# Kernel optimization log

Measured on AMD Instinct MI355X. Metric: run time of the kernel, lower is better.

## Reference

```python
import jax, jax.numpy as jnp
import numpy as np

N, E, F, H, EF, ED, L, NL, NH, OD = 2048, 65536, 128, 512, 16, 64, 5, 4, 8, 64
MAX_DEG = 64


def _ln(x, s, b):
    m = x.mean(-1, keepdims=True)
    v = x.var(-1, keepdims=True)
    return (x - m) * jax.lax.rsqrt(v + 1e-5) * s + b


def setup_inputs() -> dict:
    key = jax.random.key(0)
    ks = jax.random.split(key, 40)
    s = 0.02
    x = jax.random.normal(ks[0], (N, F), jnp.float32)
    edge_index = jax.random.randint(ks[1], (2, E), 0, N, jnp.int32)
    edge_attr = jax.random.normal(ks[2], (E, EF), jnp.float32)
    # variable-length shortest paths, padded with -1
    plen = jax.random.randint(ks[3], (N, N), 0, L + 1, jnp.int32)
    pos = jnp.arange(L, dtype=jnp.int32)
    valid = pos[None, None, :] < plen[:, :, None]
    node_paths = jnp.where(valid, jax.random.randint(ks[4], (N, N, L), 0, N, jnp.int32), -1)
    edge_paths = jnp.where(valid, jax.random.randint(ks[5], (N, N, L), 0, E, jnp.int32), -1)
    p = {
        'x': x, 'edge_index': edge_index, 'edge_attr': edge_attr,
        'node_paths': node_paths, 'edge_paths': edge_paths,
        'W_node': s * jax.random.normal(ks[6], (F, H)), 'b_node': jnp.zeros((H,)),
        'W_edge': s * jax.random.normal(ks[7], (EF, ED)), 'b_edge': jnp.zeros((ED,)),
        'z_in': s * jax.random.normal(ks[8], (MAX_DEG, H)),
        'z_out': s * jax.random.normal(ks[9], (MAX_DEG, H)),
        'b_spatial': s * jax.random.normal(ks[10], (L,)),
        'edge_vector': s * jax.random.normal(ks[11], (L, ED)),
        'ln1_s': jnp.ones((NL, H)), 'ln1_b': jnp.zeros((NL, H)),
        'Wq': s * jax.random.normal(ks[12], (NL, H, H)), 'bq': jnp.zeros((NL, H)),
        'Wk': s * jax.random.normal(ks[13], (NL, H, H)), 'bk': jnp.zeros((NL, H)),
        'Wv': s * jax.random.normal(ks[14], (NL, H, H)), 'bv': jnp.zeros((NL, H)),
        'Wo': s * jax.random.normal(ks[15], (NL, H, H)), 'bo': jnp.zeros((NL, H)),
        'ln2_s': jnp.ones((NL, H)), 'ln2_b': jnp.zeros((NL, H)),
        'W1': s * jax.random.normal(ks[16], (NL, H, H)), 'b1': jnp.zeros((NL, H)),
        'W2': s * jax.random.normal(ks[17], (NL, H, H)), 'b2': jnp.zeros((NL, H)),
        'W_out': s * jax.random.normal(ks[18], (H, OD)), 'b_out': jnp.zeros((OD,)),
    }
    return p


def reference(x, edge_index, edge_attr, node_paths, edge_paths,
              W_node, b_node, W_edge, b_edge, z_in, z_out, b_spatial, edge_vector,
              ln1_s, ln1_b, Wq, bq, Wk, bk, Wv, bv, Wo, bo,
              ln2_s, ln2_b, W1, b1, W2, b2, W_out, b_out):
    n = x.shape[0]
    dk = H // NH
    h = x @ W_node + b_node  # [N,H]
    # centrality encoding: in/out degree -> learned embeddings, clamped
    in_deg = jnp.clip(jnp.zeros((n,), jnp.int32).at[edge_index[1]].add(1), 0, MAX_DEG - 1)
    out_deg = jnp.clip(jnp.zeros((n,), jnp.int32).at[edge_index[0]].add(1), 0, MAX_DEG - 1)
    h = h + z_in[in_deg] + z_out[out_deg]
    # edge encoding: mean over path of <edge_vector[k], edge_emb[path_k]>
    e_emb = edge_attr @ W_edge + b_edge           # [E,ED]
    w = e_emb @ edge_vector.T                     # [E,L] per-position dot products
    valid_e = edge_paths >= 0
    gath = w[jnp.clip(edge_paths, 0), jnp.arange(L)[None, None, :]]  # [N,N,L]
    cnt = valid_e.sum(-1).astype(h.dtype)
    c = jnp.where(cnt > 0, (gath * valid_e).sum(-1) / jnp.maximum(cnt, 1.0), 0.0)  # [N,N]
    # spatial encoding: learned scalar per path length
    plen = (node_paths >= 0).sum(-1)
    b_sp = jnp.where(plen > 0, b_spatial[jnp.clip(plen - 1, 0, L - 1)], 0.0)  # [N,N]
    bias = b_sp + c
    scale = 1.0 / jnp.sqrt(jnp.asarray(dk, h.dtype))
    for l in range(NL):
        y = _ln(h, ln1_s[l], ln1_b[l])
        q = (y @ Wq[l] + bq[l]).reshape(n, NH, dk)
        k = (y @ Wk[l] + bk[l]).reshape(n, NH, dk)
        v = (y @ Wv[l] + bv[l]).reshape(n, NH, dk)
        scores = jnp.einsum('ihd,jhd->hij', q, k) * scale + bias[None]
        attn = jax.nn.softmax(scores, axis=-1)
        o = jnp.einsum('hij,jhd->ihd', attn, v).reshape(n, H)
        h = h + o @ Wo[l] + bo[l]
        y2 = _ln(h, ln2_s[l], ln2_b[l])
        h = h + jax.nn.gelu(y2 @ W1[l] + b1[l]) @ W2[l] + b2[l]
    return h @ W_out + b_out
```

## Files before the change

kernel.cpp:

```cpp
#include <hip/hip_runtime.h>
#include <hip/hip_bf16.h>
#include <math.h>

#define N_NODES 2048
#define NEDGE   65536
#define FDIM    128
#define HDIM    512
#define EFD     16
#define EDD     64
#define LPATH   5
#define NLAYER  4
#define NHEAD   8
#define DK      64
#define ODIM    64
#define MAXDEG  64
#define PTOT    4194304

typedef __bf16 bf16;
typedef bf16 bf16x8 __attribute__((ext_vector_type(8)));
typedef bf16 bf16x4 __attribute__((ext_vector_type(4)));
typedef float f32x4 __attribute__((ext_vector_type(4)));
typedef unsigned short u16;

__global__ __launch_bounds__(256) void k_edge_w(const float* __restrict__ ea, const float* __restrict__ We,
                                                const float* __restrict__ be, const float* __restrict__ ev,
                                                const int* __restrict__ ei, int* __restrict__ din,
                                                int* __restrict__ dout, bf16* __restrict__ wT) {
    __shared__ float sM[80];
    __shared__ float sc[8];
    int t = threadIdx.x;
    if (t < 80) {
        int i = t / 5, j = t % 5;
        float acc = 0.f;
        for (int k = 0; k < EDD; ++k) acc += We[i * EDD + k] * ev[j * EDD + k];
        sM[t] = acc;
    } else if (t >= 128 && t < 128 + LPATH) {
        int j = t - 128;
        float acc = 0.f;
        for (int k = 0; k < EDD; ++k) acc += be[k] * ev[j * EDD + k];
        sc[j] = acc;
    }
    int e = blockIdx.x * 256 + t;
    atomicAdd(&dout[ei[e]], 1);
    atomicAdd(&din[ei[NEDGE + e]], 1);
    __syncthreads();
    const float4* p = (const float4*)(ea + (size_t)e * EFD);
    float4 a0 = p[0], a1 = p[1], a2 = p[2], a3 = p[3];
    float a[16] = {a0.x, a0.y, a0.z, a0.w, a1.x, a1.y, a1.z, a1.w,
                   a2.x, a2.y, a2.z, a2.w, a3.x, a3.y, a3.z, a3.w};
    float out[LPATH];
#pragma unroll
    for (int j = 0; j < LPATH; ++j) out[j] = sc[j];
#pragma unroll
    for (int i = 0; i < 16; ++i)
#pragma unroll
        for (int j = 0; j < LPATH; ++j) out[j] += a[i] * sM[i * LPATH + j];
#pragma unroll
    for (int j = 0; j < LPATH; ++j) wT[(size_t)j * NEDGE + e] = (bf16)out[j];
}

__global__ __launch_bounds__(1024) void k_bias3(const int* __restrict__ ep, const bf16* __restrict__ wT,
                                                const float* __restrict__ bsp, bf16* __restrict__ bias) {
    __shared__ char lds[163840];
    int t = threadIdx.x;
    size_t basep = (size_t)blockIdx.x * 8192;
    bf16x8 pre[4];
#pragma unroll
    for (int u = 0; u < 4; ++u) pre[u] = *(const bf16x8*)(wT + u * 8192 + t * 8);
    int* ish = (int*)lds;
    const int4* src = (const int4*)(ep + basep * 5);
#pragma unroll
    for (int u = 0; u < 10; ++u) ((int4*)ish)[t + 1024 * u] = src[t + 1024 * u];
    __syncthreads();
    unsigned pa[8], pb[8], pc[8];
#pragma unroll
    for (int r = 0; r < 8; ++r) {
        int p5 = (r * 1024 + t) * 5;
        int e0 = ish[p5], e1 = ish[p5 + 1], e2 = ish[p5 + 2], e3 = ish[p5 + 3], e4 = ish[p5 + 4];
        unsigned mk = (unsigned)(e0 >= 0) | ((unsigned)(e1 >= 0) << 1) | ((unsigned)(e2 >= 0) << 2)
                    | ((unsigned)(e3 >= 0) << 3) | ((unsigned)(e4 >= 0) << 4);
        pa[r] = ((unsigned)e0 & 0xFFFFu) | ((unsigned)e1 << 16);
        pb[r] = ((unsigned)e2 & 0xFFFFu) | ((unsigned)e3 << 16);
        pc[r] = ((unsigned)e4 & 0xFFFFu) | (mk << 16);
    }
    __syncthreads();
    {
        bf16* b0 = (bf16*)lds;
#pragma unroll
        for (int u = 0; u < 4; ++u) *(bf16x8*)(b0 + u * 8192 + t * 8) = pre[u];
    }
    __syncthreads();
    float csum[8] = {};
    int cur = 0;
#pragma unroll
    for (int s = 0; s < 10; ++s) {
        int l = s >> 1, half = s & 1;
        bf16x8 nxt[4];
        if (s < 9) {
            const bf16* wn = wT + (size_t)((s + 1) >> 1) * NEDGE + ((s + 1) & 1) * 32768;
#pragma unroll
            for (int u = 0; u < 4; ++u) nxt[u] = *(const bf16x8*)(wn + u * 8192 + t * 8);
        }
        const bf16* bc = (const bf16*)lds + cur * 32768;
#pragma unroll
        for (int r = 0; r < 8; ++r) {
            unsigned ix = (l == 0) ? (pa[r] & 0xFFFFu) : (l == 1) ? (pa[r] >> 16)
                        : (l == 2) ? (pb[r] & 0xFFFFu) : (l == 3) ? (pb[r] >> 16) : (pc[r] & 0xFFFFu);
            bool hit = (((pc[r] >> (16 + l)) & 1u) != 0) && ((ix >> 15) == (unsigned)half);
            if (hit) csum[r] += (float)bc[ix & 32767u];
        }
        __syncthreads();
        if (s < 9) {
            bf16* ba = (bf16*)lds + (cur ^ 1) * 32768;
#pragma unroll
            for (int u = 0; u < 4; ++u) *(bf16x8*)(ba + u * 8192 + t * 8) = nxt[u];
            cur ^= 1;
        }
        __syncthreads();
    }
#pragma unroll
    for (int r = 0; r < 8; ++r) {
        int cnt = __popc((int)((pc[r] >> 16) & 0x1Fu));
        float b = cnt ? bsp[cnt - 1] + csum[r] / (float)cnt : 0.f;
        bias[basep + r * 1024 + t] = (bf16)b;
    }
}

__global__ __launch_bounds__(256) void k_ln(const float* __restrict__ h, const float* __restrict__ sc,
                                            const float* __restrict__ bi, bf16* __restrict__ y) {
    int t = threadIdx.x, w = t >> 6, l = t & 63;
    int row = blockIdx.x * 4 + w;
    const float* hp = h + (size_t)row * HDIM + l * 8;
    float4 a = *(const float4*)hp;
    float4 b = *(const float4*)(hp + 4);
    float s = a.x + a.y + a.z + a.w + b.x + b.y + b.z + b.w;
    float q = a.x * a.x + a.y * a.y + a.z * a.z + a.w * a.w
            + b.x * b.x + b.y * b.y + b.z * b.z + b.w * b.w;
#pragma unroll
    for (int m = 1; m < 64; m <<= 1) { s += __shfl_xor(s, m); q += __shfl_xor(q, m); }
    float mean = s * (1.f / HDIM);
    float var = q * (1.f / HDIM) - mean * mean;
    float r = rsqrtf(var + 1e-5f);
    float4 s0 = *(const float4*)(sc + l * 8), s1 = *(const float4*)(sc + l * 8 + 4);
    float4 b0 = *(const float4*)(bi + l * 8), b1 = *(const float4*)(bi + l * 8 + 4);
    float va[8] = {a.x, a.y, a.z, a.w, b.x, b.y, b.z, b.w};
    float ss[8] = {s0.x, s0.y, s0.z, s0.w, s1.x, s1.y, s1.z, s1.w};
    float bb[8] = {b0.x, b0.y, b0.z, b0.w, b1.x, b1.y, b1.z, b1.w};
    bf16x8 o;
#pragma unroll
    for (int c = 0; c < 8; ++c) o[c] = (bf16)((va[c] - mean) * r * ss[c] + bb[c]);
    *(bf16x8*)(y + (size_t)row * HDIM + l * 8) = o;
}

__global__ __launch_bounds__(256) void k_wprep(const float* __restrict__ Wq, const float* __restrict__ Wk,
                                               const float* __restrict__ Wv, const float* __restrict__ Wo,
                                               const float* __restrict__ W1, const float* __restrict__ W2,
                                               const float* __restrict__ Wn, const float* __restrict__ Wout,
                                               bf16* __restrict__ Wt, bf16* __restrict__ WnT,
                                               bf16* __restrict__ WoutT) {
    __shared__ float Ls[64][68];
    int m = blockIdx.y;
    int q = blockIdx.x;
    int t = threadIdx.x;
    int rr = t >> 4, cc = t & 15;
    int nl = t >> 2, kc = t & 3;
    if (m < 24) {
        int lay = m / 6, type = m % 6;
        const float* src = type == 0 ? Wq : type == 1 ? Wk : type == 2 ? Wv : type == 3 ? Wo : type == 4 ? W1 : W2;
        src += (size_t)lay * (HDIM * HDIM);
        int tk = q >> 3, tn = q & 7;
#pragma unroll
        for (int u = 0; u < 4; ++u) {
            float4 v = *(const float4*)(src + (size_t)(tk * 64 + rr + 16 * u) * HDIM + tn * 64 + cc * 4);
            *(float4*)&Ls[rr + 16 * u][cc * 4] = v;
        }
        __syncthreads();
        bf16 tmp[16];
#pragma unroll
        for (int u = 0; u < 16; ++u) tmp[u] = (bf16)Ls[kc * 16 + u][nl];
        bf16* dst = Wt + (size_t)m * (HDIM * HDIM) + (size_t)(tn * 64 + nl) * HDIM + tk * 64 + kc * 16;
        *(bf16x8*)(dst) = *(bf16x8*)&tmp[0];
        *(bf16x8*)(dst + 8) = *(bf16x8*)&tmp[8];
    } else if (m == 24) {
        if (q >= 16) return;
        int tk = q >> 3, tn = q & 7;
#pragma unroll
        for (int u = 0; u < 4; ++u) {
            float4 v = *(const float4*)(Wn + (size_t)(tk * 64 + rr + 16 * u) * HDIM + tn * 64 + cc * 4);
            *(float4*)&Ls[rr + 16 * u][cc * 4] = v;
        }
        __syncthreads();
        bf16 tmp[16];
#pragma unroll
        for (int u = 0; u < 16; ++u) tmp[u] = (bf16)Ls[kc * 16 + u][nl];
        bf16* dst = WnT + (size_t)(tn * 64 + nl) * FDIM + tk * 64 + kc * 16;
        *(bf16x8*)dst = *(bf16x8*)&tmp[0];
        *(bf16x8*)(dst + 8) = *(bf16x8*)&tmp[8];
    } else {
        if (q >= 8) return;
        int tk = q;
#pragma unroll
        for (int u = 0; u < 4; ++u) {
            float4 v = *(const float4*)(Wout + (size_t)(tk * 64 + rr + 16 * u) * ODIM + cc * 4);
            *(float4*)&Ls[rr + 16 * u][cc * 4] = v;
        }
        __syncthreads();
        bf16 tmp[16];
#pragma unroll
        for (int u = 0; u < 16; ++u) tmp[u] = (bf16)Ls[kc * 16 + u][nl];
        bf16* dst = WoutT + (size_t)nl * HDIM + tk * 64 + kc * 16;
        *(bf16x8*)dst = *(bf16x8*)&tmp[0];
        *(bf16x8*)(dst + 8) = *(bf16x8*)&tmp[8];
    }
}

__global__ __launch_bounds__(256) void k_nmm(const float* __restrict__ x, const bf16* __restrict__ Bt,
                                             const float* __restrict__ bn, const float* __restrict__ zin,
                                             const float* __restrict__ zout, const int* __restrict__ din,
                                             const int* __restrict__ dout, float* __restrict__ h) {
    __shared__ bf16 Bs[8192];
    int t = threadIdx.x, w = t >> 6, l = t & 63, lr = l & 15, lg = l >> 4;
    int j0 = blockIdx.x * 64, i0 = blockIdx.y * 64;
    const bf16* Bp = Bt + (size_t)j0 * FDIM;
#pragma unroll
    for (int rnd = 0; rnd < 4; ++rnd) {
        int tt = rnd * 256 + t;
        int ks = tt >> 8, qq = (tt >> 6) & 3, mm = (tt >> 2) & 15, gg = tt & 3;
        *(bf16x8*)(Bs + tt * 8) = *(const bf16x8*)(Bp + (size_t)(qq * 16 + mm) * FDIM + ks * 32 + gg * 8);
    }
    __syncthreads();
    const float* ap = x + (size_t)(i0 + w * 16 + lr) * FDIM + 8 * lg;
    f32x4 acc[4] = {};
#pragma unroll
    for (int ks = 0; ks < 4; ++ks) {
        float4 f0 = *(const float4*)(ap + ks * 32);
        float4 f1 = *(const float4*)(ap + ks * 32 + 4);
        bf16x8 a;
        a[0] = (bf16)f0.x; a[1] = (bf16)f0.y; a[2] = (bf16)f0.z; a[3] = (bf16)f0.w;
        a[4] = (bf16)f1.x; a[5] = (bf16)f1.y; a[6] = (bf16)f1.z; a[7] = (bf16)f1.w;
        const bf16* bb = Bs + ks * 2048 + lr * 32 + lg * 8;
#pragma unroll
        for (int sub = 0; sub < 4; ++sub)
            acc[sub] = __builtin_amdgcn_mfma_f32_16x16x32_bf16(a, *(const bf16x8*)(bb + sub * 512), acc[sub], 0, 0, 0);
    }
#pragma unroll
    for (int r = 0; r < 4; ++r) {
        int i = i0 + w * 16 + lg * 4 + r;
        int di = min(din[i], MAXDEG - 1), dz = min(dout[i], MAXDEG - 1);
#pragma unroll
        for (int sub = 0; sub < 4; ++sub) {
            int j = j0 + sub * 16 + lr;
            h[(size_t)i * HDIM + j] = acc[sub][r] + bn[j] + zin[(size_t)di * HDIM + j] + zout[(size_t)dz * HDIM + j];
        }
    }
}

__global__ __launch_bounds__(256) void k_qkv(const bf16* __restrict__ A, const bf16* __restrict__ Wt_l,
                                             const float* __restrict__ bq, const float* __restrict__ bk,
                                             const float* __restrict__ bv, bf16* __restrict__ qf,
                                             bf16* __restrict__ kf, bf16* __restrict__ vf) {
    __shared__ bf16 Bs[16384];
    int t = threadIdx.x, w = t >> 6, l = t & 63, lr = l & 15, lg = l >> 4;
    int j0 = blockIdx.x * 32, i0 = blockIdx.y * 64;
    int type = j0 >> 9, n0 = j0 & 511;
    const bf16* Bp = Wt_l + (size_t)type * (HDIM * HDIM) + (size_t)n0 * HDIM;
#pragma unroll
    for (int rnd = 0; rnd < 8; ++rnd) {
        int tt = rnd * 256 + t;
        int ks = tt >> 7, qq = (tt >> 6) & 1, mm = (tt >> 2) & 15, gg = tt & 3;
        bf16x8 v = *(const bf16x8*)(Bp + (size_t)(qq * 16 + mm) * HDIM + ks * 32 + gg * 8);
        *(bf16x8*)(Bs + tt * 8) = v;
    }
    __syncthreads();
    const bf16* ap = A + (size_t)(i0 + w * 16 + lr) * HDIM + 8 * lg;
    const float* bvec = (type == 0 ? bq : type == 1 ? bk : bv);
    f32x4 acc[2] = {};
#pragma unroll 4
    for (int ks = 0; ks < 16; ++ks) {
        bf16x8 a  = *(const bf16x8*)(ap + ks * 32);
        const bf16* bb = Bs + ks * 1024 + lr * 32 + lg * 8;
        bf16x8 b0 = *(const bf16x8*)(bb);
        bf16x8 b1 = *(const bf16x8*)(bb + 512);
        acc[0] = __builtin_amdgcn_mfma_f32_16x16x32_bf16(a, b0, acc[0], 0, 0, 0);
        acc[1] = __builtin_amdgcn_mfma_f32_16x16x32_bf16(a, b1, acc[1], 0, 0, 0);
    }
    int h = n0 >> 6;
    if (type < 2) {
        bf16* dst = (type == 0 ? qf : kf);
        int hf = (n0 & 32) >> 5;
        float sc = (type == 0 ? 0.125f : 1.0f);
#pragma unroll
        for (int sub = 0; sub < 2; ++sub) {
#pragma unroll
            for (int r = 0; r < 4; ++r) {
                int i = i0 + w * 16 + lg * 4 + r;
                float v = (acc[sub][r] + bvec[n0 + sub * 16 + lr]) * sc;
                int lgp = sub * 2 + (lr >> 3);
                size_t off = (((size_t)(h * 128 + (i >> 4)) * 2 + hf) << 9) + lgp * 128 + (lg * 4 + r) * 8 + (lr & 7);
                dst[off] = (bf16)v;
            }
        }
    } else {
#pragma unroll
        for (int sub = 0; sub < 2; ++sub) {
#pragma unroll
            for (int r = 0; r < 4; ++r) {
                int node = i0 + w * 16 + lg * 4 + r;
                int dd = (n0 & 63) + sub * 16 + lr;
                float v = acc[sub][r] + bvec[n0 + sub * 16 + lr];
                size_t off = (((size_t)(h * 4 + (dd >> 4)) * 64 + (node >> 5)) << 9)
                           + ((node >> 3) & 3) * 128 + (dd & 15) * 8 + (node & 7);
                vf[off] = (bf16)v;
            }
        }
    }
}

#define FL_RES   1
#define FL_GELU  2
#define FL_OUTF  4

__device__ inline float gelu_f(float x) {
    float x3 = x * x * x;
    float u = 0.7978845608028654f * (x + 0.044715f * x3);
    return 0.5f * x * (1.f + tanhf(u));
}

__global__ __launch_bounds__(1024) void k_mm(const bf16* __restrict__ A, const bf16* __restrict__ Bt,
                                             const float* __restrict__ bvec, const float* __restrict__ res,
                                             float* __restrict__ outF, bf16* __restrict__ outB, int flags) {
    __shared__ bf16 Bs[32768];
    __shared__ float Osh[4][16][68];
    int t = threadIdx.x, w = t >> 6, l = t & 63, lr = l & 15, lg = l >> 4;
    int ti = w & 3, s = w >> 2;
    int j0 = blockIdx.x * 64, i0 = blockIdx.y * 64;
    const bf16* Bp = Bt + (size_t)j0 * HDIM;
#pragma unroll
    for (int rnd = 0; rnd < 4; ++rnd) {
        int tt = rnd * 1024 + t;
        int ks = tt >> 8, qq = (tt >> 6) & 3, mm = (tt >> 2) & 15, gg = tt & 3;
        bf16x8 v = *(const bf16x8*)(Bp + (size_t)(qq * 16 + mm) * HDIM + ks * 32 + gg * 8);
        *(bf16x8*)(Bs + tt * 8) = v;
    }
    __syncthreads();
    const bf16* ap = A + (size_t)(i0 + ti * 16 + lr) * HDIM + 8 * lg;
    f32x4 acc[4] = {};
#pragma unroll
    for (int kk = 0; kk < 4; ++kk) {
        int ks = s * 4 + kk;
        bf16x8 a = *(const bf16x8*)(ap + ks * 32);
        const bf16* bb = Bs + ks * 2048 + lr * 32 + lg * 8;
#pragma unroll
        for (int sub = 0; sub < 4; ++sub) {
            bf16x8 b = *(const bf16x8*)(bb + sub * 512);
            acc[sub] = __builtin_amdgcn_mfma_f32_16x16x32_bf16(a, b, acc[sub], 0, 0, 0);
        }
    }
    if (s == 0) {
#pragma unroll
        for (int sub = 0; sub < 4; ++sub)
#pragma unroll
            for (int r = 0; r < 4; ++r) Osh[ti][lg * 4 + r][sub * 16 + lr] = acc[sub][r];
    }
    __syncthreads();
    if (s == 1) {
#pragma unroll
        for (int sub = 0; sub < 4; ++sub)
#pragma unroll
            for (int r = 0; r < 4; ++r) Osh[ti][lg * 4 + r][sub * 16 + lr] += acc[sub][r];
    }
    __syncthreads();
    if (s == 2) {
#pragma unroll
        for (int sub = 0; sub < 4; ++sub)
#pragma unroll
            for (int r = 0; r < 4; ++r) Osh[ti][lg * 4 + r][sub * 16 + lr] += acc[sub][r];
    }
    __syncthreads();
    if (s == 3) {
#pragma unroll
        for (int sub = 0; sub < 4; ++sub) {
#pragma unroll
            for (int r = 0; r < 4; ++r) {
                int i = i0 + ti * 16 + lg * 4 + r;
                int j = j0 + sub * 16 + lr;
                float v = Osh[ti][lg * 4 + r][sub * 16 + lr] + acc[sub][r] + bvec[j];
                if (flags & FL_RES) v += res[(size_t)i * HDIM + j];
                if (flags & FL_GELU) v = gelu_f(v);
                if (flags & FL_OUTF) outF[(size_t)i * HDIM + j] = v;
                else outB[(size_t)i * HDIM + j] = (bf16)v;
            }
        }
    }
}

__global__ __launch_bounds__(1024) void k_mmln(const float* __restrict__ h, const bf16* __restrict__ Bt,
                                               const float* __restrict__ lnS, const float* __restrict__ lnB,
                                               const float* __restrict__ bvec, bf16* __restrict__ outB) {
    __shared__ bf16 As[32768];
    __shared__ bf16 Bs[32768];
    __shared__ float Osh[4][16][68];
    __shared__ float sbuf[HDIM], bbuf[HDIM];
    int t = threadIdx.x, w = t >> 6, l = t & 63, lr = l & 15, lg = l >> 4;
    int ti = w & 3, s = w >> 2;
    int j0 = blockIdx.x * 64, i0 = blockIdx.y * 64;
    if (t < HDIM) sbuf[t] = lnS[t];
    else bbuf[t - HDIM] = lnB[t - HDIM];
    const bf16* Bp = Bt + (size_t)j0 * HDIM;
#pragma unroll
    for (int rnd = 0; rnd < 4; ++rnd) {
        int tt = rnd * 1024 + t;
        int ks = tt >> 8, qq = (tt >> 6) & 3, mm = (tt >> 2) & 15, gg = tt & 3;
        *(bf16x8*)(Bs + tt * 8) = *(const bf16x8*)(Bp + (size_t)(qq * 16 + mm) * HDIM + ks * 32 + gg * 8);
    }
    int row = t >> 4, ksc = t & 15;
    const float* hp = h + (size_t)(i0 + row) * HDIM + ksc * 32;
    float4 hv[8];
    float S = 0.f, Q = 0.f;
#pragma unroll
    for (int u = 0; u < 8; ++u) {
        hv[u] = *(const float4*)(hp + u * 4);
        S += hv[u].x + hv[u].y + hv[u].z + hv[u].w;
        Q += hv[u].x * hv[u].x + hv[u].y * hv[u].y + hv[u].z * hv[u].z + hv[u].w * hv[u].w;
    }
#pragma unroll
    for (int m = 1; m < 16; m <<= 1) { S += __shfl_xor(S, m); Q += __shfl_xor(Q, m); }
    float mean = S * (1.f / HDIM);
    float var = Q * (1.f / HDIM) - mean * mean;
    float rr = rsqrtf(var + 1e-5f);
    float ca = rr, cc = -mean * rr;
    __syncthreads();
    {
        bf16 tmp[32];
#pragma unroll
        for (int u = 0; u < 8; ++u) {
            float vv[4] = {hv[u].x, hv[u].y, hv[u].z, hv[u].w};
#pragma unroll
            for (int c = 0; c < 4; ++c) {
                int col = ksc * 32 + u * 4 + c;
                tmp[u * 4 + c] = (bf16)(fmaf(fmaf(vv[c], ca, cc), sbuf[col], bbuf[col]));
            }
        }
        bf16* dst = As + (row >> 4) * 8192 + ksc * 512 + (row & 15) * 32;
#pragma unroll
        for (int u = 0; u < 4; ++u) *(bf16x8*)(dst + u * 8) = *(bf16x8*)&tmp[u * 8];
    }
    __syncthreads();
    const bf16* apl = As + ti * 8192 + lr * 32 + lg * 8;
    f32x4 acc[4] = {};
#pragma unroll
    for (int kk = 0; kk < 4; ++kk) {
        int ks = s * 4 + kk;
        bf16x8 a = *(const bf16x8*)(apl + ks * 512);
        const bf16* bb = Bs + ks * 2048 + lr * 32 + lg * 8;
#pragma unroll
        for (int sub = 0; sub < 4; ++sub)
            acc[sub] = __builtin_amdgcn_mfma_f32_16x16x32_bf16(a, *(const bf16x8*)(bb + sub * 512), acc[sub], 0, 0, 0);
    }
    if (s == 0) {
#pragma unroll
        for (int sub = 0; sub < 4; ++sub)
#pragma unroll
            for (int r = 0; r < 4; ++r) Osh[ti][lg * 4 + r][sub * 16 + lr] = acc[sub][r];
    }
    __syncthreads();
    if (s == 1) {
#pragma unroll
        for (int sub = 0; sub < 4; ++sub)
#pragma unroll
            for (int r = 0; r < 4; ++r) Osh[ti][lg * 4 + r][sub * 16 + lr] += acc[sub][r];
    }
    __syncthreads();
    if (s == 2) {
#pragma unroll
        for (int sub = 0; sub < 4; ++sub)
#pragma unroll
            for (int r = 0; r < 4; ++r) Osh[ti][lg * 4 + r][sub * 16 + lr] += acc[sub][r];
    }
    __syncthreads();
    if (s == 3) {
#pragma unroll
        for (int sub = 0; sub < 4; ++sub) {
#pragma unroll
            for (int r = 0; r < 4; ++r) {
                int i = i0 + ti * 16 + lg * 4 + r;
                int j = j0 + sub * 16 + lr;
                float v = gelu_f(Osh[ti][lg * 4 + r][sub * 16 + lr] + acc[sub][r] + bvec[j]);
                outB[(size_t)i * HDIM + j] = (bf16)v;
            }
        }
    }
}

__global__ __launch_bounds__(1024) void k_attn2(const bf16* __restrict__ qf, const bf16* __restrict__ kf,
                                                const bf16* __restrict__ vf, const bf16* __restrict__ biasb,
                                                bf16* __restrict__ ob) {
    __shared__ char Pb[16 * 1024];
    __shared__ float Osh[4][64][17];
    __shared__ float Msh[4][4][16], Lsh[4][4][16];
    int t = threadIdx.x, w = t >> 6, l = t & 63, lr = l & 15, lg = l >> 4;
    int ti = w & 3, s = w >> 2;
    int bid = blockIdx.x;
    int wid = (bid & 7) * 32 + (bid >> 3);
    int i0 = (wid >> 3) * 64, hh = wid & 7;
    int irow = i0 + ti * 16;

    const bf16* qb = qf + (((size_t)(hh * 128 + (irow >> 4)) * 2) << 9) + l * 8;
    bf16x8 qy0 = *(const bf16x8*)(qb);
    bf16x8 qy1 = *(const bf16x8*)(qb + 512);

    char* pwr = Pb + w * 1024 + lr * 64;
    unsigned kx = (unsigned)(lr & 6) << 3;

    float m_run = -3e38f, l_run = 0.f;
    f32x4 oacc[4] = {};

    int jb0 = s * 512;
    const bf16* kbp = kf + (((size_t)(hh * 128 + (jb0 >> 4)) * 2) << 9) + l * 8;
    bf16x8 ka0 = *(const bf16x8*)(kbp);
    bf16x8 ka1 = *(const bf16x8*)(kbp + 512);
    bf16x8 ka2 = *(const bf16x8*)(kbp + 1024);
    bf16x8 ka3 = *(const bf16x8*)(kbp + 1536);
    const bf16* bpp = biasb + (size_t)(irow + lr) * N_NODES + jb0 + lg * 4;
    bf16x4 ba0 = *(const bf16x4*)(bpp);
    bf16x4 ba1 = *(const bf16x4*)(bpp + 16);

    for (int it = 0; it < 16; ++it) {
        int jb = s * 512 + it * 32;
        const bf16* vb = vf + (((size_t)(hh * 4) * 64 + (jb >> 5)) << 9) + l * 8;
        bf16x8 vx0 = *(const bf16x8*)(vb);
        bf16x8 vx1 = *(const bf16x8*)(vb + 32768);
        bf16x8 vx2 = *(const bf16x8*)(vb + 65536);
        bf16x8 vx3 = *(const bf16x8*)(vb + 98304);
        bf16x8 kn0, kn1, kn2, kn3;
        bf16x4 bn0, bn1;
        if (it < 15) {
            int jn = jb + 32;
            const bf16* kbn = kf + (((size_t)(hh * 128 + (jn >> 4)) * 2) << 9) + l * 8;
            kn0 = *(const bf16x8*)(kbn);
            kn1 = *(const bf16x8*)(kbn + 512);
            kn2 = *(const bf16x8*)(kbn + 1024);
            kn3 = *(const bf16x8*)(kbn + 1536);
            const bf16* bpn = biasb + (size_t)(irow + lr) * N_NODES + jn + lg * 4;
            bn0 = *(const bf16x4*)(bpn);
            bn1 = *(const bf16x4*)(bpn + 16);
        }

        f32x4 s0v = {}, s1v = {};
        __builtin_amdgcn_s_setprio(1);
        s0v = __builtin_amdgcn_mfma_f32_16x16x32_bf16(ka0, qy0, s0v, 0, 0, 0);
        s0v = __builtin_amdgcn_mfma_f32_16x16x32_bf16(ka1, qy1, s0v, 0, 0, 0);
        s1v = __builtin_amdgcn_mfma_f32_16x16x32_bf16(ka2, qy0, s1v, 0, 0, 0);
        s1v = __builtin_amdgcn_mfma_f32_16x16x32_bf16(ka3, qy1, s1v, 0, 0, 0);
        __builtin_amdgcn_s_setprio(0);

        float p0[4], p1[4];
        float mt = -3e38f;
#pragma unroll
        for (int r = 0; r < 4; ++r) {
            p0[r] = s0v[r] + (float)ba0[r];
            p1[r] = s1v[r] + (float)ba1[r];
            mt = fmaxf(mt, fmaxf(p0[r], p1[r]));
        }
        mt = fmaxf(mt, __shfl_xor(mt, 16));
        mt = fmaxf(mt, __shfl_xor(mt, 32));
        if (!__all(mt <= m_run + 8.f)) {
            float mn = fmaxf(m_run, mt);
            float alpha = __expf(m_run - mn);
            l_run *= alpha;
#pragma unroll
            for (int d = 0; d < 4; ++d) oacc[d] *= alpha;
            m_run = mn;
        }
        float ps = 0.f;
        bf16x4 pk0, pk1;
#pragma unroll
        for (int r = 0; r < 4; ++r) {
            p0[r] = __expf(p0[r] - m_run);
            p1[r] = __expf(p1[r] - m_run);
            ps += p0[r] + p1[r];
            pk0[r] = (bf16)p0[r];
            pk1[r] = (bf16)p1[r];
        }
        ps += __shfl_xor(ps, 16);
        ps += __shfl_xor(ps, 32);
        l_run += ps;

        *(bf16x4*)(pwr + ((lg * 8) ^ kx)) = pk0;
        *(bf16x4*)(pwr + ((32 + lg * 8) ^ kx)) = pk1;
        asm volatile("s_waitcnt lgkmcnt(0)" ::: "memory");
        __builtin_amdgcn_sched_barrier(0x20);
        bf16x8 py = *(bf16x8*)(Pb + w * 1024 + lr * 64 + ((lg * 16) ^ kx));
        __builtin_amdgcn_s_setprio(1);
        oacc[0] = __builtin_amdgcn_mfma_f32_16x16x32_bf16(vx0, py, oacc[0], 0, 0, 0);
        oacc[1] = __builtin_amdgcn_mfma_f32_16x16x32_bf16(vx1, py, oacc[1], 0, 0, 0);
        oacc[2] = __builtin_amdgcn_mfma_f32_16x16x32_bf16(vx2, py, oacc[2], 0, 0, 0);
        oacc[3] = __builtin_amdgcn_mfma_f32_16x16x32_bf16(vx3, py, oacc[3], 0, 0, 0);
        __builtin_amdgcn_s_setprio(0);
        ka0 = kn0; ka1 = kn1; ka2 = kn2; ka3 = kn3;
        ba0 = bn0; ba1 = bn1;
    }

    __syncthreads();
    if (lg == 0) { Msh[ti][s][lr] = m_run; Lsh[ti][s][lr] = l_run; }
    __syncthreads();
    float m0 = Msh[ti][0][lr], m1 = Msh[ti][1][lr], m2 = Msh[ti][2][lr], m3 = Msh[ti][3][lr];
    float mtot = fmaxf(fmaxf(m0, m1), fmaxf(m2, m3));
    float l_tot = Lsh[ti][0][lr] * __expf(m0 - mtot) + Lsh[ti][1][lr] * __expf(m1 - mtot)
                + Lsh[ti][2][lr] * __expf(m2 - mtot) + Lsh[ti][3][lr] * __expf(m3 - mtot);
    float fac = __expf(m_run - mtot);
#pragma unroll
    for (int d = 0; d < 4; ++d) oacc[d] *= fac;
    if (s == 0) {
#pragma unroll
        for (int db = 0; db < 4; ++db)
#pragma unroll
            for (int r = 0; r < 4; ++r) Osh[ti][db * 16 + lg * 4 + r][lr] = oacc[db][r];
    }
    __syncthreads();
    if (s == 1) {
#pragma unroll
        for (int db = 0; db < 4; ++db)
#pragma unroll
            for (int r = 0; r < 4; ++r) Osh[ti][db * 16 + lg * 4 + r][lr] += oacc[db][r];
    }
    __syncthreads();
    if (s == 2) {
#pragma unroll
        for (int db = 0; db < 4; ++db)
#pragma unroll
            for (int r = 0; r < 4; ++r) Osh[ti][db * 16 + lg * 4 + r][lr] += oacc[db][r];
    }
    __syncthreads();
    if (s == 3) {
        float inv = 1.f / l_tot;
#pragma unroll
        for (int db = 0; db < 4; ++db) {
            bf16x4 o4;
#pragma unroll
            for (int r = 0; r < 4; ++r)
                o4[r] = (bf16)((Osh[ti][db * 16 + lg * 4 + r][lr] + oacc[db][r]) * inv);
            *(bf16x4*)(ob + (size_t)(irow + lr) * HDIM + hh * DK + db * 16 + lg * 4) = o4;
        }
    }
}

__global__ __launch_bounds__(256) void k_fout(const float* __restrict__ h, const bf16* __restrict__ Bt,
                                              const float* __restrict__ bvec, float* __restrict__ C) {
    __shared__ float Osh[16][68];
    int t = threadIdx.x, s = t >> 6, l = t & 63, lr = l & 15, lg = l >> 4;
    int i0 = blockIdx.x * 16;
    const float* ap = h + (size_t)(i0 + lr) * HDIM + s * 128 + lg * 8;
    f32x4 acc[4] = {};
#pragma unroll
    for (int kk = 0; kk < 4; ++kk) {
        float4 f0 = *(const float4*)(ap + kk * 32);
        float4 f1 = *(const float4*)(ap + kk * 32 + 4);
        bf16x8 a;
        a[0] = (bf16)f0.x; a[1] = (bf16)f0.y; a[2] = (bf16)f0.z; a[3] = (bf16)f0.w;
        a[4] = (bf16)f1.x; a[5] = (bf16)f1.y; a[6] = (bf16)f1.z; a[7] = (bf16)f1.w;
#pragma unroll
        for (int sub = 0; sub < 4; ++sub) {
            bf16x8 b = *(const bf16x8*)(Bt + (size_t)(sub * 16 + lr) * HDIM + s * 128 + kk * 32 + lg * 8);
            acc[sub] = __builtin_amdgcn_mfma_f32_16x16x32_bf16(a, b, acc[sub], 0, 0, 0);
        }
    }
    if (s == 0) {
#pragma unroll
        for (int sub = 0; sub < 4; ++sub)
#pragma unroll
            for (int r = 0; r < 4; ++r) Osh[lg * 4 + r][sub * 16 + lr] = acc[sub][r];
    }
    __syncthreads();
    if (s == 1) {
#pragma unroll
        for (int sub = 0; sub < 4; ++sub)
#pragma unroll
            for (int r = 0; r < 4; ++r) Osh[lg * 4 + r][sub * 16 + lr] += acc[sub][r];
    }
    __syncthreads();
    if (s == 2) {
#pragma unroll
        for (int sub = 0; sub < 4; ++sub)
#pragma unroll
            for (int r = 0; r < 4; ++r) Osh[lg * 4 + r][sub * 16 + lr] += acc[sub][r];
    }
    __syncthreads();
    if (s == 3) {
#pragma unroll
        for (int sub = 0; sub < 4; ++sub) {
#pragma unroll
            for (int r = 0; r < 4; ++r) {
                int i = i0 + lg * 4 + r;
                int j = sub * 16 + lr;
                C[(size_t)i * ODIM + j] = Osh[lg * 4 + r][sub * 16 + lr] + acc[sub][r] + bvec[j];
            }
        }
    }
}

extern "C" void kernel_launch(void* const* d_in, const int* in_sizes, int n_in,
                              void* d_out, int out_size, void* d_ws, size_t ws_size,
                              hipStream_t stream) {
    const float* x      = (const float*)d_in[0];
    const int*   ei     = (const int*)d_in[1];
    const float* eattr  = (const float*)d_in[2];
    const int*   epaths = (const int*)d_in[4];
    const float* Wn     = (const float*)d_in[5];
    const float* bn     = (const float*)d_in[6];
    const float* We     = (const float*)d_in[7];
    const float* be     = (const float*)d_in[8];
    const float* zin    = (const float*)d_in[9];
    const float* zout   = (const float*)d_in[10];
    const float* bsp    = (const float*)d_in[11];
    const float* ev     = (const float*)d_in[12];
    const float* ln1s   = (const float*)d_in[13];
    const float* ln1b   = (const float*)d_in[14];
    const float* Wq     = (const float*)d_in[15];
    const float* bq     = (const float*)d_in[16];
    const float* Wk     = (const float*)d_in[17];
    const float* bk     = (const float*)d_in[18];
    const float* Wv     = (const float*)d_in[19];
    const float* bv     = (const float*)d_in[20];
    const float* Wo     = (const float*)d_in[21];
    const float* bo     = (const float*)d_in[22];
    const float* ln2s   = (const float*)d_in[23];
    const float* ln2b   = (const float*)d_in[24];
    const float* W1     = (const float*)d_in[25];
    const float* b1     = (const float*)d_in[26];
    const float* W2     = (const float*)d_in[27];
    const float* b2     = (const float*)d_in[28];
    const float* Wout   = (const float*)d_in[29];
    const float* bout   = (const float*)d_in[30];

    char* base = (char*)d_ws;
    size_t off = 0;
    auto alloc = [&](size_t bytes) { char* p = base + off; off = (off + bytes + 255) & ~(size_t)255; return p; };
    bf16*  bias   = (bf16*)alloc((size_t)N_NODES * N_NODES * 2);
    float* h      = (float*)alloc((size_t)N_NODES * HDIM * 4);
    bf16*  wT     = (bf16*)alloc((size_t)LPATH * NEDGE * 2);
    int*   deg    = (int*)alloc(2 * N_NODES * 4);
    bf16*  WnT    = (bf16*)alloc((size_t)HDIM * FDIM * 2);
    bf16*  WoutT  = (bf16*)alloc((size_t)ODIM * HDIM * 2);
    bf16*  Wt     = (bf16*)alloc((size_t)NLAYER * 6 * HDIM * HDIM * 2);
    bf16*  y_bf   = (bf16*)alloc((size_t)N_NODES * HDIM * 2);
    bf16*  qfb    = (bf16*)alloc((size_t)NHEAD * 128 * 2 * 512 * 2);
    bf16*  kfb    = (bf16*)alloc((size_t)NHEAD * 128 * 2 * 512 * 2);
    bf16*  vfb    = (bf16*)alloc((size_t)NHEAD * 4 * 64 * 512 * 2);
    bf16*  ob_bf  = (bf16*)alloc((size_t)N_NODES * HDIM * 2);
    bf16*  t1_bf  = (bf16*)alloc((size_t)N_NODES * HDIM * 2);
    int* din = deg;
    int* dout = deg + N_NODES;

    hipMemsetAsync(deg, 0, 2 * N_NODES * sizeof(int), stream);

    k_edge_w<<<NEDGE / 256, 256, 0, stream>>>(eattr, We, be, ev, ei, din, dout, wT);
    k_bias3<<<512, 1024, 0, stream>>>(epaths, wT, bsp, bias);
    k_wprep<<<dim3(64, 26), 256, 0, stream>>>(Wq, Wk, Wv, Wo, W1, W2, Wn, Wout, Wt, WnT, WoutT);
    k_nmm<<<dim3(8, 32), 256, 0, stream>>>(x, WnT, bn, zin, zout, din, dout, h);

    dim3 gqkv(48, 32);
    dim3 gmm(8, 32);

    for (int lay = 0; lay < NLAYER; ++lay) {
        const bf16* Wt_l = Wt + (size_t)lay * 6 * HDIM * HDIM;
        size_t bOff = (size_t)lay * HDIM;
        k_ln<<<512, 256, 0, stream>>>(h, ln1s + bOff, ln1b + bOff, y_bf);
        k_qkv<<<gqkv, 256, 0, stream>>>(y_bf, Wt_l, bq + bOff, bk + bOff, bv + bOff, qfb, kfb, vfb);
        k_attn2<<<256, 1024, 0, stream>>>(qfb, kfb, vfb, bias, ob_bf);
        k_mm<<<gmm, 1024, 0, stream>>>(ob_bf, Wt_l + (size_t)3 * HDIM * HDIM, bo + bOff, h, h, nullptr, FL_RES | FL_OUTF);
        k_mmln<<<gmm, 1024, 0, stream>>>(h, Wt_l + (size_t)4 * HDIM * HDIM, ln2s + bOff, ln2b + bOff, b1 + bOff, t1_bf);
        k_mm<<<gmm, 1024, 0, stream>>>(t1_bf, Wt_l + (size_t)5 * HDIM * HDIM, b2 + bOff, h, h, nullptr, FL_RES | FL_OUTF);
    }
    k_fout<<<128, 256, 0, stream>>>(h, WoutT, bout, (float*)d_out);
}
```

Before: 462.5 us.

## Fold log2e into Q scale and bias; process two path chunks per bias block

```diff
diff --git a/kernel.cpp b/kernel.cpp
--- a/kernel.cpp
+++ b/kernel.cpp
@@ -15,6 +15,7 @@
 #define ODIM    64
 #define MAXDEG  64
 #define PTOT    4194304
+#define LOG2E   1.4426950408889634f
 
 typedef __bf16 bf16;
 typedef bf16 bf16x8 __attribute__((ext_vector_type(8)));
@@ -63,66 +64,86 @@
                                                 const float* __restrict__ bsp, bf16* __restrict__ bias) {
     __shared__ char lds[163840];
     int t = threadIdx.x;
-    size_t basep = (size_t)blockIdx.x * 8192;
-    bf16x8 pre[4];
-#pragma unroll
-    for (int u = 0; u < 4; ++u) pre[u] = *(const bf16x8*)(wT + u * 8192 + t * 8);
+    size_t basep = (size_t)blockIdx.x * 16384;
+    bf16x8 pre[8];
+#pragma unroll
+    for (int u = 0; u < 8; ++u) pre[u] = *(const bf16x8*)(wT + u * 8192 + t * 8);
     int* ish = (int*)lds;
-    const int4* src = (const int4*)(ep + basep * 5);
-#pragma unroll
-    for (int u = 0; u < 10; ++u) ((int4*)ish)[t + 1024 * u] = src[t + 1024 * u];
-    __syncthreads();
-    unsigned pa[8], pb[8], pc[8];
+    {
+        const int4* src = (const int4*)(ep + basep * 5);
+#pragma unroll
+        for (int u = 0; u < 10; ++u) ((int4*)ish)[t + 1024 * u] = src[t + 1024 * u];
+    }
+    __syncthreads();
+    unsigned pa0[8], pb0[8], pc0[8];
 #pragma unroll
     for (int r = 0; r < 8; ++r) {
         int p5 = (r * 1024 + t) * 5;
         int e0 = ish[p5], e1 = ish[p5 + 1], e2 = ish[p5 + 2], e3 = ish[p5 + 3], e4 = ish[p5 + 4];
         unsigned mk = (unsigned)(e0 >= 0) | ((unsigned)(e1 >= 0) << 1) | ((unsigned)(e2 >= 0) << 2)
                     | ((unsigned)(e3 >= 0) << 3) | ((unsigned)(e4 >= 0) << 4);
-        pa[r] = ((unsigned)e0 & 0xFFFFu) | ((unsigned)e1 << 16);
-        pb[r] = ((unsigned)e2 & 0xFFFFu) | ((unsigned)e3 << 16);
-        pc[r] = ((unsigned)e4 & 0xFFFFu) | (mk << 16);
+        pa0[r] = ((unsigned)e0 & 0xFFFFu) | ((unsigned)e1 << 16);
+        pb0[r] = ((unsigned)e2 & 0xFFFFu) | ((unsigned)e3 << 16);
+        pc0[r] = ((unsigned)e4 & 0xFFFFu) | (mk << 16);
     }
     __syncthreads();
     {
-        bf16* b0 = (bf16*)lds;
-#pragma unroll
-        for (int u = 0; u < 4; ++u) *(bf16x8*)(b0 + u * 8192 + t * 8) = pre[u];
-    }
-    __syncthreads();
-    float csum[8] = {};
-    int cur = 0;
-#pragma unroll
-    for (int s = 0; s < 10; ++s) {
-        int l = s >> 1, half = s & 1;
-        bf16x8 nxt[4];
-        if (s < 9) {
-            const bf16* wn = wT + (size_t)((s + 1) >> 1) * NEDGE + ((s + 1) & 1) * 32768;
-#pragma unroll
-            for (int u = 0; u < 4; ++u) nxt[u] = *(const bf16x8*)(wn + u * 8192 + t * 8);
-        }
-        const bf16* bc = (const bf16*)lds + cur * 32768;
+        const int4* src = (const int4*)(ep + (basep + 8192) * 5);
+#pragma unroll
+        for (int u = 0; u < 10; ++u) ((int4*)ish)[t + 1024 * u] = src[t + 1024 * u];
+    }
+    __syncthreads();
+    unsigned pa1[8], pb1[8], pc1[8];
+#pragma unroll
+    for (int r = 0; r < 8; ++r) {
+        int p5 = (r * 1024 + t) * 5;
+        int e0 = ish[p5], e1 = ish[p5 + 1], e2 = ish[p5 + 2], e3 = ish[p5 + 3], e4 = ish[p5 + 4];
+        unsigned mk = (unsigned)(e0 >= 0) | ((unsigned)(e1 >= 0) << 1) | ((unsigned)(e2 >= 0) << 2)
+                    | ((unsigned)(e3 >= 0) << 3) | ((unsigned)(e4 >= 0) << 4);
+        pa1[r] = ((unsigned)e0 & 0xFFFFu) | ((unsigned)e1 << 16);
+        pb1[r] = ((unsigned)e2 & 0xFFFFu) | ((unsigned)e3 << 16);
+        pc1[r] = ((unsigned)e4 & 0xFFFFu) | (mk << 16);
+    }
+    __syncthreads();
+    bf16* wsl = (bf16*)lds;
+#pragma unroll
+    for (int u = 0; u < 8; ++u) *(bf16x8*)(wsl + u * 8192 + t * 8) = pre[u];
+    __syncthreads();
+    float cs0[8] = {}, cs1[8] = {};
+#pragma unroll
+    for (int l = 0; l < LPATH; ++l) {
+        bf16x8 nxt[8];
+        if (l < 4) {
+            const bf16* wn = wT + (size_t)(l + 1) * NEDGE;
+#pragma unroll
+            for (int u = 0; u < 8; ++u) nxt[u] = *(const bf16x8*)(wn + u * 8192 + t * 8);
+        }
 #pragma unroll
         for (int r = 0; r < 8; ++r) {
-            unsigned ix = (l == 0) ? (pa[r] & 0xFFFFu) : (l == 1) ? (pa[r] >> 16)
-                        : (l == 2) ? (pb[r] & 0xFFFFu) : (l == 3) ? (pb[r] >> 16) : (pc[r] & 0xFFFFu);
-            bool hit = (((pc[r] >> (16 + l)) & 1u) != 0) && ((ix >> 15) == (unsigned)half);
-            if (hit) csum[r] += (float)bc[ix & 32767u];
+            unsigned ix0 = (l == 0) ? (pa0[r] & 0xFFFFu) : (l == 1) ? (pa0[r] >> 16)
+                         : (l == 2) ? (pb0[r] & 0xFFFFu) : (l == 3) ? (pb0[r] >> 16) : (pc0[r] & 0xFFFFu);
+            unsigned ix1 = (l == 0) ? (pa1[r] & 0xFFFFu) : (l == 1) ? (pa1[r] >> 16)
+                         : (l == 2) ? (pb1[r] & 0xFFFFu) : (l == 3) ? (pb1[r] >> 16) : (pc1[r] & 0xFFFFu);
+            float v0 = (float)wsl[ix0 & 0xFFFFu];
+            float v1 = (float)wsl[ix1 & 0xFFFFu];
+            cs0[r] += ((pc0[r] >> (16 + l)) & 1u) ? v0 : 0.f;
+            cs1[r] += ((pc1[r] >> (16 + l)) & 1u) ? v1 : 0.f;
         }
         __syncthreads();
-        if (s < 9) {
-            bf16* ba = (bf16*)lds + (cur ^ 1) * 32768;
-#pragma unroll
-            for (int u = 0; u < 4; ++u) *(bf16x8*)(ba + u * 8192 + t * 8) = nxt[u];
-            cur ^= 1;
+        if (l < 4) {
+#pragma unroll
+            for (int u = 0; u < 8; ++u) *(bf16x8*)(wsl + u * 8192 + t * 8) = nxt[u];
         }
         __syncthreads();
     }
 #pragma unroll
     for (int r = 0; r < 8; ++r) {
-        int cnt = __popc((int)((pc[r] >> 16) & 0x1Fu));
-        float b = cnt ? bsp[cnt - 1] + csum[r] / (float)cnt : 0.f;
-        bias[basep + r * 1024 + t] = (bf16)b;
+        int c0 = __popc((int)((pc0[r] >> 16) & 0x1Fu));
+        int c1 = __popc((int)((pc1[r] >> 16) & 0x1Fu));
+        float b0 = c0 ? (bsp[c0 - 1] + cs0[r] / (float)c0) * LOG2E : 0.f;
+        float b1 = c1 ? (bsp[c1 - 1] + cs1[r] / (float)c1) * LOG2E : 0.f;
+        bias[basep + r * 1024 + t] = (bf16)b0;
+        bias[basep + 8192 + r * 1024 + t] = (bf16)b1;
     }
 }
 
@@ -288,7 +309,7 @@
     if (type < 2) {
         bf16* dst = (type == 0 ? qf : kf);
         int hf = (n0 & 32) >> 5;
-        float sc = (type == 0 ? 0.125f : 1.0f);
+        float sc = (type == 0 ? 0.125f * LOG2E : 1.0f);
 #pragma unroll
         for (int sub = 0; sub < 2; ++sub) {
 #pragma unroll
@@ -564,9 +585,9 @@
         }
         mt = fmaxf(mt, __shfl_xor(mt, 16));
         mt = fmaxf(mt, __shfl_xor(mt, 32));
-        if (!__all(mt <= m_run + 8.f)) {
+        if (!__all(mt <= m_run + 11.5416f)) {
             float mn = fmaxf(m_run, mt);
-            float alpha = __expf(m_run - mn);
+            float alpha = exp2f(m_run - mn);
             l_run *= alpha;
 #pragma unroll
             for (int d = 0; d < 4; ++d) oacc[d] *= alpha;
@@ -576,8 +597,8 @@
         bf16x4 pk0, pk1;
 #pragma unroll
         for (int r = 0; r < 4; ++r) {
-            p0[r] = __expf(p0[r] - m_run);
-            p1[r] = __expf(p1[r] - m_run);
+            p0[r] = exp2f(p0[r] - m_run);
+            p1[r] = exp2f(p1[r] - m_run);
             ps += p0[r] + p1[r];
             pk0[r] = (bf16)p0[r];
             pk1[r] = (bf16)p1[r];
@@ -606,9 +627,9 @@
     __syncthreads();
     float m0 = Msh[ti][0][lr], m1 = Msh[ti][1][lr], m2 = Msh[ti][2][lr], m3 = Msh[ti][3][lr];
     float mtot = fmaxf(fmaxf(m0, m1), fmaxf(m2, m3));
-    float l_tot = Lsh[ti][0][lr] * __expf(m0 - mtot) + Lsh[ti][1][lr] * __expf(m1 - mtot)
-                + Lsh[ti][2][lr] * __expf(m2 - mtot) + Lsh[ti][3][lr] * __expf(m3 - mtot);
-    float fac = __expf(m_run - mtot);
+    float l_tot = Lsh[ti][0][lr] * exp2f(m0 - mtot) + Lsh[ti][1][lr] * exp2f(m1 - mtot)
+                + Lsh[ti][2][lr] * exp2f(m2 - mtot) + Lsh[ti][3][lr] * exp2f(m3 - mtot);
+    float fac = exp2f(m_run - mtot);
 #pragma unroll
     for (int d = 0; d < 4; ++d) oacc[d] *= fac;
     if (s == 0) {
@@ -755,7 +776,7 @@
     hipMemsetAsync(deg, 0, 2 * N_NODES * sizeof(int), stream);
 
     k_edge_w<<<NEDGE / 256, 256, 0, stream>>>(eattr, We, be, ev, ei, din, dout, wT);
-    k_bias3<<<512, 1024, 0, stream>>>(epaths, wT, bsp, bias);
+    k_bias3<<<256, 1024, 0, stream>>>(epaths, wT, bsp, bias);
     k_wprep<<<dim3(64, 26), 256, 0, stream>>>(Wq, Wk, Wv, Wo, W1, W2, Wn, Wout, Wt, WnT, WoutT);
     k_nmm<<<dim3(8, 32), 256, 0, stream>>>(x, WnT, bn, zin, zout, din, dout, h);
 
```

Result: no change. 462.4 us (-0.0%).
